# Kernel optimization log

Hardware: AMD Instinct MI355X
Metric: run time of the kernel (lower is better)

The kernel has to match this reference:

```python
import jax, jax.numpy as jnp
import numpy as np

NUM_CLIP_VIT_FEAT = 576  # default kwarg of mixed_mask


def _mixed_mask(pad_ends, full_starts, full_ends, bt2i, blm, B, S):
    # Faithful translation of OmniAttentionMechanism.mixed_mask evaluated over
    # all (b, q_idx, kv_idx). Note python operator precedence: & binds tighter
    # than ^, so the original expression is (A&t2i) ^ (B&C&lm) ^ (D&mmu).
    q_idx = jnp.arange(S)[:, None]          # [S,1]
    kv_idx = jnp.arange(S)[None, :]         # [1,S]
    causal_qk = q_idx >= kv_idx             # [S,S]
    # kv_idx < pad_ends[b, kv_idx]  ->  arange(S) < pad_ends  (per batch row)
    pad_region = jnp.arange(S) < pad_ends   # [B,S] over kv
    causal = (~pad_region)[:, None, :] & causal_qk[None]              # [B,S,S]
    # full block: kv in [full_starts[q], full_ends[q])
    full = (kv_idx < full_ends[:, None]) & (kv_idx >= full_starts[:, None])  # [S,S]
    eye = q_idx == kv_idx                                             # [S,S]
    t2i = eye[None] ^ (causal | full[None])                           # [B,S,S]
    lm = causal_qk                                                    # [S,S]
    mmu = causal_qk | (kv_idx <= NUM_CLIP_VIT_FEAT + 3)               # [S,S]
    b = jnp.arange(B)[:, None, None]
    mask = ((b < bt2i) & t2i) \
         ^ ((b >= bt2i) & (b < bt2i + blm) & lm[None]) \
         ^ ((b >= bt2i + blm) & mmu[None])
    return mask  # [B,S,S] bool


def setup_inputs() -> dict:
    key = jax.random.key(0)
    B_T2I, B_LM, B_MMU = 4, 4, 4
    B, H, S, D = B_T2I + B_LM + B_MMU, 8, 1024, 64
    k1, k2, k3 = jax.random.split(key, 3)
    q = jax.random.normal(k1, (B, H, S, D), jnp.float32)
    k = jax.random.normal(k2, (B, H, S, D), jnp.float32)
    v = jax.random.normal(k3, (B, H, S, D), jnp.float32)

    # full_starts/full_ends from image_begin_ends=[(512,1024)]
    full_starts = np.arange(S)
    full_ends = np.arange(S)
    for ib, ie in [(512, 1024)]:
        full_starts[ib:ie] = ib
        full_ends[ib:ie] = ie

    # pad_ends from default pad_begin_ends=[(0,256),(0,300),(0,400),(0,0)]
    pad_ends = np.tile(np.arange(S), (B, 1))
    for cnt, (pb, pe) in enumerate([(0, 256), (0, 300), (0, 400), (0, 0)]):
        pad_ends[cnt, pb:pe] = pe

    return {
        "q": q, "k": k, "v": v,
        "pad_ends": jnp.asarray(pad_ends, jnp.int32),
        "full_starts": jnp.asarray(full_starts, jnp.int32),
        "full_ends": jnp.asarray(full_ends, jnp.int32),
        "batch_size_t2i": B_T2I,
        "batch_size_lm": B_LM,
    }


def reference(q, k, v, pad_ends, full_starts, full_ends, batch_size_t2i, batch_size_lm):
    B, H, S, D = q.shape
    mask = _mixed_mask(pad_ends, full_starts, full_ends,
                       batch_size_t2i, batch_size_lm, B, S)      # [B,S,S]
    scale = 1.0 / jnp.sqrt(jnp.asarray(D, q.dtype))
    scores = jnp.einsum('bhqd,bhkd->bhqk', q, k) * scale          # [B,H,S,S]
    scores = jnp.where(mask[:, None], scores, jnp.asarray(-1e30, scores.dtype))
    attn = jax.nn.softmax(scores, axis=-1)
    return jnp.einsum('bhqk,bhkd->bhqd', attn, v)
```

## Files before the change

### kernel.cpp

```cpp
#include <hip/hip_runtime.h>


typedef __attribute__((ext_vector_type(8))) short short8;
typedef __attribute__((ext_vector_type(4))) float floatx4;
typedef __attribute__((ext_vector_type(4))) unsigned int uint4v;

#define S_LEN 1024
#define D_DIM 64
#define H_NUM 8
#define B_NUM 12
#define BT2I_CONST 4
#define BLM_CONST 4
#define NUM_CLIP_P3 579
#define KV_ELEMS (B_NUM * H_NUM * S_LEN * D_DIM)
#define P_EPS 7.888609052210118e-31f

__device__ __forceinline__ float bf2f(short s) {
    unsigned int u = ((unsigned int)(unsigned short)s) << 16;
    return __builtin_bit_cast(float, u);
}
__device__ __forceinline__ short f2bf(float f) {
    unsigned int u = __builtin_bit_cast(unsigned int, f);
    unsigned int r = (u + 0x7fffu + ((u >> 16) & 1u)) >> 16;
    return (short)(unsigned short)r;
}
__device__ __forceinline__ short scale_bf(short x) {
    float f = bf2f(x) * 0.125f;
    return (short)(unsigned short)(__builtin_bit_cast(unsigned int, f) >> 16);
}
__device__ __forceinline__ int detect_bf16(const unsigned int* q) {
    int l = threadIdx.x & 63;
    unsigned int w = q[l];
    unsigned int e = (w >> 7) & 0xffu;
    bool sane = (e >= 100u && e <= 140u);
    unsigned long long m = __ballot(sane);
    return (__popcll(m) > 32) ? 1 : 0;
}

__global__ __launch_bounds__(256)
void preprocess_kv(const void* __restrict__ Kv, const void* __restrict__ Vv,
                   const unsigned int* __restrict__ Qw,
                   short* __restrict__ Kf, short* __restrict__ Vf) {
    __shared__ __align__(16) short Ls[64][72];
    const int is_bf16 = detect_bf16(Qw);
    const int x = blockIdx.x;
    const int kind = x & 1;
    const int kt = (x >> 1) & 15;
    const int bh = x >> 5;
    const int t = threadIdx.x;
    const long long base = (long long)bh * S_LEN * D_DIM + (long long)kt * 64 * D_DIM;
    const void* Src = kind ? Vv : Kv;

    #pragma unroll
    for (int j = 0; j < 4; ++j) {
        int lin = j * 1024 + t * 4;
        int row = lin >> 6, col = lin & 63;
        long long src = base + (long long)row * D_DIM + col;
        short v0, v1, v2, v3;
        if (is_bf16) {
            const short* p = (const short*)Src + src;
            v0 = p[0]; v1 = p[1]; v2 = p[2]; v3 = p[3];
        } else {
            floatx4 f = *(const floatx4*)((const float*)Src + src);
            v0 = f2bf(f[0]); v1 = f2bf(f[1]); v2 = f2bf(f[2]); v3 = f2bf(f[3]);
        }
        if (kind == 0) {
            Ls[row][col] = v0; Ls[row][col + 1] = v1;
            Ls[row][col + 2] = v2; Ls[row][col + 3] = v3;
        } else {
            Ls[col][row] = v0; Ls[col + 1][row] = v1;
            Ls[col + 2][row] = v2; Ls[col + 3][row] = v3;
        }
    }
    __syncthreads();

    short* dst = (kind ? Vf : Kf) + ((long long)bh * 16 + kt) * 4096;
    #pragma unroll
    for (int rep = 0; rep < 2; ++rep) {
        int idx = rep * 256 + t;
        int g = idx >> 6, lam = idx & 63;
        int gg = g >> 1, hh = g & 1, q = lam >> 4, l16 = lam & 15;
        short8 v = *(const short8*)&Ls[gg * 16 + l16][hh * 32 + q * 8];
        *(short8*)(dst + (g * 64 + lam) * 8) = v;
    }
}

__global__ __launch_bounds__(64, 2)
void omni_attn_main(const void* __restrict__ Qv, const int* __restrict__ pad_ends,
                    const int* __restrict__ fstarts, const int* __restrict__ fends,
                    const short* __restrict__ Kf, const short* __restrict__ Vf,
                    float* __restrict__ Out) {
    const int lid = blockIdx.x;
    const int h = lid & 7;
    const int s = lid >> 3;
    const int b = s >> 6;
    const int su = s & 63;
    const int qu = (su + 5 * b) & 63;
    const int qb0 = qu * 16;

    const int t = threadIdx.x;
    const int l = t & 63;
    const int lane16 = l & 15;
    const int quad = l >> 4;

    const int is_bf16 = detect_bf16((const unsigned int*)Qv);
    const int cls = (b < BT2I_CONST) ? 0 : ((b < BT2I_CONST + BLM_CONST) ? 1 : 2);
    const int bh = b * H_NUM + h;
    const long long base = (long long)bh * S_LEN * D_DIM;
    const int qmax_blk = qb0 + 15;

    unsigned int apmask = 0u;
    int fnp = 0x7fffffff;
    if (cls == 0) {
        #pragma unroll
        for (int kt = 0; kt < 16; ++kt) {
            int kg = kt * 64 + l;
            bool nonpad = (kg >= pad_ends[b * S_LEN + kg]);
            unsigned long long m = __ballot(nonpad);
            apmask |= (m == 0ull ? 1u : 0u) << kt;
            int cand = m ? (kt * 64 + __builtin_ctzll(m)) : 0x7fffffff;
            fnp = min(fnp, cand);
        }
    }
    const bool risky = (cls == 0) && (fnp >= qb0) && (fnp <= qmax_blk);

    int fs_min, fe_max;
    {
        int fsv = fstarts[qb0 + lane16];
        int fev = fends[qb0 + lane16];
        #pragma unroll
        for (int off = 1; off < 16; off <<= 1) {
            fsv = min(fsv, __shfl_xor(fsv, off, 64));
            fev = max(fev, __shfl_xor(fev, off, 64));
        }
        fs_min = fsv; fe_max = fev;
    }

    unsigned int keepmask = 0u;
    #pragma unroll
    for (int kt = 0; kt < 16; ++kt) {
        const int kvbase = kt * 64;
        bool keep;
        if (cls == 0) {
            bool allpad = ((apmask >> kt) & 1u) != 0u;
            keep = risky ||
                   ((kvbase < fe_max) && (kvbase + 64 > fs_min)) ||
                   ((kvbase <= qmax_blk) && (!allpad || (kvbase + 63 >= qb0)));
        } else if (cls == 1) {
            keep = (kvbase <= qmax_blk);
        } else {
            keep = (kvbase <= qmax_blk) || (kvbase <= NUM_CLIP_P3);
        }
        keepmask |= (keep ? 1u : 0u) << kt;
    }

    short8 aq[2];
    {
        const int row = qb0 + lane16;
        if (is_bf16) {
            const short8* qp = (const short8*)((const short*)Qv + base
                                               + (long long)row * D_DIM + quad * 8);
            short8 r0 = qp[0], r1 = qp[4];
            #pragma unroll
            for (int jj = 0; jj < 8; ++jj) {
                aq[0][jj] = scale_bf(r0[jj]);
                aq[1][jj] = scale_bf(r1[jj]);
            }
        } else {
            const floatx4* qp = (const floatx4*)((const float*)Qv + base
                                                 + (long long)row * D_DIM + quad * 8);
            floatx4 f0 = qp[0], f1 = qp[1], f2 = qp[8], f3 = qp[9];
            #pragma unroll
            for (int jj = 0; jj < 4; ++jj) {
                aq[0][jj]     = f2bf(f0[jj] * 0.125f);
                aq[0][4 + jj] = f2bf(f1[jj] * 0.125f);
                aq[1][jj]     = f2bf(f2[jj] * 0.125f);
                aq[1][4 + jj] = f2bf(f3[jj] * 0.125f);
            }
        }
    }

    const int qvl = qb0 + lane16;
    const int fsl = fstarts[qvl];
    const int fel = fends[qvl];
    int fsmax, femin;
    {
        int a = fsl, e = fel;
        #pragma unroll
        for (int off = 1; off < 16; off <<= 1) {
            a = max(a, __shfl_xor(a, off, 64));
            e = min(e, __shfl_xor(e, off, 64));
        }
        fsmax = a; femin = e;
    }

    floatx4 Oc[4];
    float lsum = 0.f;
    #pragma unroll
    for (int c = 0; c < 4; ++c) Oc[c] = (floatx4){0.f, 0.f, 0.f, 0.f};

    const short* Kfb = Kf + (long long)bh * (16 * 4096);
    const short* Vfb = Vf + (long long)bh * (16 * 4096);

    short8 kkf[4][2];
    short8 vvf[4][2];

    auto load_K = [&](int kt) {
        const short8* p = (const short8*)(Kfb + (long long)kt * 4096);
        #pragma unroll
        for (int f = 0; f < 4; ++f)
            #pragma unroll
            for (int hh = 0; hh < 2; ++hh)
                kkf[f][hh] = p[(f * 2 + hh) * 64 + l];
    };
    auto load_V = [&](int kt) {
        const short8* p = (const short8*)(Vfb + (long long)kt * 4096);
        #pragma unroll
        for (int c = 0; c < 4; ++c)
            #pragma unroll
            for (int hh = 0; hh < 2; ++hh)
                vvf[c][hh] = p[(c * 2 + hh) * 64 + l];
    };

    unsigned int mrem = keepmask;
    int kt = __builtin_ctz(mrem); mrem &= mrem - 1;
    load_K(kt); load_V(kt);
    int pev = 0;
    if (cls == 0) pev = pad_ends[b * S_LEN + kt * 64 + l];
    for (;;) {
        int ktN = -1;
        if (mrem) { ktN = __builtin_ctz(mrem); mrem &= mrem - 1; }

        const int kvbase = kt * 64;
        unsigned long long pm = 0ull;
        if (cls == 0) {
            pm = __ballot((kvbase + l) >= pev);
            if (ktN >= 0) pev = pad_ends[b * S_LEN + ktN * 64 + l];
        }

        floatx4 sc[4];
        #pragma unroll
        for (int f = 0; f < 4; ++f) {
            floatx4 c = (floatx4){0.f, 0.f, 0.f, 0.f};
            c = __builtin_amdgcn_mfma_f32_16x16x32_bf16(kkf[f][0], aq[0], c, 0, 0, 0);
            c = __builtin_amdgcn_mfma_f32_16x16x32_bf16(kkf[f][1], aq[1], c, 0, 0, 0);
            sc[f] = c;
        }
        bool fast;
        if (cls == 0) {
            bool np_all  = (pm == ~0ull);
            bool below   = (kvbase + 63 < qb0);
            bool eyefree = below || (kvbase > qb0 + 15);
            fast = (np_all && below) ||
                   (eyefree && (kvbase >= fsmax) && (kvbase + 64 <= femin));
        } else if (cls == 1) {
            fast = (kvbase + 63 <= qb0);
        } else {
            fast = (kvbase + 63 <= qb0) || (kvbase + 63 <= NUM_CLIP_P3);
        }
        if (!fast) {
            const int q = qvl;
            #pragma unroll
            for (int f = 0; f < 4; ++f) {
                #pragma unroll
                for (int r = 0; r < 4; ++r) {
                    const int k = kvbase + f * 16 + 4 * quad + r;
                    bool m;
                    if (cls == 0) {
                        bool knp    = ((pm >> (f * 16 + 4 * quad + r)) & 1ull) != 0ull;
                        bool causal = knp && (q >= k);
                        bool full   = (k >= fsl) && (k < fel);
                        m = (q == k) != (causal || full);
                    } else if (cls == 1) {
                        m = (q >= k);
                    } else {
                        m = (q >= k) || (k <= NUM_CLIP_P3);
                    }
                    sc[f][r] = m ? sc[f][r] : -1e30f;
                }
            }
        }
        unsigned int uu[4][2];
        float ls = 0.f;
        #pragma unroll
        for (int f = 0; f < 4; ++f) {
            float p0 = __expf(sc[f][0]) + P_EPS;
            float p1 = __expf(sc[f][1]) + P_EPS;
            float p2 = __expf(sc[f][2]) + P_EPS;
            float p3 = __expf(sc[f][3]) + P_EPS;
            ls += p0 + p1 + p2 + p3;
            asm("v_cvt_pk_bf16_f32 %0, %1, %2" : "=v"(uu[f][0]) : "v"(p0), "v"(p1));
            asm("v_cvt_pk_bf16_f32 %0, %1, %2" : "=v"(uu[f][1]) : "v"(p2), "v"(p3));
        }
        lsum += ls;
        short8 pa[2];
        #pragma unroll
        for (int hh = 0; hh < 2; ++hh) {
            unsigned int x0 = uu[2 * hh][0],     y0 = uu[2 * hh + 1][0];
            unsigned int x1 = uu[2 * hh][1],     y1 = uu[2 * hh + 1][1];
            asm("v_permlane32_swap_b32 %0, %1" : "+v"(x0), "+v"(y0));
            asm("v_permlane16_swap_b32 %0, %1" : "+v"(x0), "+v"(y0));
            asm("v_permlane32_swap_b32 %0, %1" : "+v"(x1), "+v"(y1));
            asm("v_permlane16_swap_b32 %0, %1" : "+v"(x1), "+v"(y1));
            uint4v w;
            w[0] = x0; w[1] = x1; w[2] = y0; w[3] = y1;
            pa[hh] = __builtin_bit_cast(short8, w);
        }

        if (ktN >= 0) load_K(ktN);

        #pragma unroll
        for (int c = 0; c < 4; ++c) {
            Oc[c] = __builtin_amdgcn_mfma_f32_16x16x32_bf16(pa[0], vvf[c][0], Oc[c], 0, 0, 0);
            Oc[c] = __builtin_amdgcn_mfma_f32_16x16x32_bf16(pa[1], vvf[c][1], Oc[c], 0, 0, 0);
        }

        if (ktN >= 0) load_V(ktN);
        if (ktN < 0) break;
        kt = ktN;
    }

    {
        float sv0 = lsum;
        sv0 += __shfl_xor(sv0, 16, 64);
        sv0 += __shfl_xor(sv0, 32, 64);
        float* ob = Out + ((long long)bh * S_LEN + qb0) * D_DIM;
        #pragma unroll
        for (int r = 0; r < 4; ++r) {
            float sv = __shfl(sv0, quad * 4 + r, 64);
            float inv = 1.0f / sv;
            #pragma unroll
            for (int c = 0; c < 4; ++c)
                ob[(quad * 4 + r) * D_DIM + c * 16 + lane16] = Oc[c][r] * inv;
        }
    }
}

__global__ __launch_bounds__(256)
void omni_attn_fallback(const void* __restrict__ Qv, const void* __restrict__ Kv,
                        const void* __restrict__ Vv, const int* __restrict__ pad_ends,
                        const int* __restrict__ fstarts, const int* __restrict__ fends,
                        float* __restrict__ Out) {
    __shared__ short Ks[64][72];
    __shared__ short Vts[64][72];
    __shared__ short Ps[4][16][72];
    __shared__ int   padv[64];
    const int qt = blockIdx.x, h = blockIdx.y, b = blockIdx.z;
    const int t = threadIdx.x, wq = t >> 6, l = t & 63;
    const int lane16 = l & 15, quad = l >> 4;
    const int is_bf16 = detect_bf16((const unsigned int*)Qv);
    const int cls = (b < BT2I_CONST) ? 0 : ((b < BT2I_CONST + BLM_CONST) ? 1 : 2);
    const int bh = b * H_NUM + h;
    const long long base = (long long)bh * S_LEN * D_DIM;
    const short* Kb16 = (const short*)Kv + base;
    const short* Vb16 = (const short*)Vv + base;
    const float* Kbf = (const float*)Kv + base;
    const float* Vbf = (const float*)Vv + base;
    const int qbase = qt * 64 + wq * 16;
    short8 aq0, aq1;
    if (is_bf16) {
        const short8* qp = (const short8*)((const short*)Qv + base + (qbase + lane16) * D_DIM + quad * 8);
        short8 r0 = qp[0], r1 = qp[4];
        #pragma unroll
        for (int jj = 0; jj < 8; ++jj) { aq0[jj] = scale_bf(r0[jj]); aq1[jj] = scale_bf(r1[jj]); }
    } else {
        const floatx4* qp = (const floatx4*)((const float*)Qv + base + (qbase + lane16) * D_DIM + quad * 8);
        floatx4 f0 = qp[0], f1 = qp[1], f2 = qp[8], f3 = qp[9];
        #pragma unroll
        for (int jj = 0; jj < 4; ++jj) {
            aq0[jj] = f2bf(f0[jj] * 0.125f); aq0[4 + jj] = f2bf(f1[jj] * 0.125f);
            aq1[jj] = f2bf(f2[jj] * 0.125f); aq1[4 + jj] = f2bf(f3[jj] * 0.125f);
        }
    }
    int qg[4], fs[4], fe[4];
    #pragma unroll
    for (int r = 0; r < 4; ++r) {
        qg[r] = qbase + quad * 4 + r; fs[r] = fstarts[qg[r]]; fe[r] = fends[qg[r]];
    }
    floatx4 Oc[4];
    #pragma unroll
    for (int c = 0; c < 4; ++c) Oc[c] = (floatx4){0.f, 0.f, 0.f, 0.f};
    float m_i[4] = {-1e30f, -1e30f, -1e30f, -1e30f};
    float l_i[4] = {0.f, 0.f, 0.f, 0.f};
    for (int kt = 0; kt < S_LEN / 64; ++kt) {
        const int kvbase = kt * 64;
        __syncthreads();
        {
            const int kvr = t >> 2, seg = t & 3;
            if (is_bf16) {
                const short8* gk = (const short8*)(Kb16 + (kvbase + kvr) * D_DIM);
                *(short8*)&Ks[kvr][seg * 8] = gk[seg];
                *(short8*)&Ks[kvr][(seg + 4) * 8] = gk[seg + 4];
                const short8* gv = (const short8*)(Vb16 + (kvbase + kvr) * D_DIM);
                short8 v0 = gv[seg], v1 = gv[seg + 4];
                #pragma unroll
                for (int jj = 0; jj < 8; ++jj) {
                    Vts[seg * 8 + jj][kvr] = v0[jj];
                    Vts[32 + seg * 8 + jj][kvr] = v1[jj];
                }
            } else {
                const floatx4* gk = (const floatx4*)(Kbf + (kvbase + kvr) * D_DIM);
                floatx4 k0 = gk[seg * 2], k1 = gk[seg * 2 + 1];
                floatx4 k2 = gk[8 + seg * 2], k3 = gk[8 + seg * 2 + 1];
                #pragma unroll
                for (int jj = 0; jj < 4; ++jj) {
                    Ks[kvr][seg * 8 + jj] = f2bf(k0[jj]);
                    Ks[kvr][seg * 8 + 4 + jj] = f2bf(k1[jj]);
                    Ks[kvr][32 + seg * 8 + jj] = f2bf(k2[jj]);
                    Ks[kvr][32 + seg * 8 + 4 + jj] = f2bf(k3[jj]);
                }
                const floatx4* gv = (const floatx4*)(Vbf + (kvbase + kvr) * D_DIM);
                floatx4 v0 = gv[seg * 2], v1 = gv[seg * 2 + 1];
                floatx4 v2 = gv[8 + seg * 2], v3 = gv[8 + seg * 2 + 1];
                #pragma unroll
                for (int jj = 0; jj < 4; ++jj) {
                    Vts[seg * 8 + jj][kvr] = f2bf(v0[jj]);
                    Vts[seg * 8 + 4 + jj][kvr] = f2bf(v1[jj]);
                    Vts[32 + seg * 8 + jj][kvr] = f2bf(v2[jj]);
                    Vts[32 + seg * 8 + 4 + jj][kvr] = f2bf(v3[jj]);
                }
            }
            if (t < 64) {
                int kg = kvbase + t;
                padv[t] = (kg < pad_ends[b * S_LEN + kg]) ? 1 : 0;
            }
        }
        __syncthreads();
        floatx4 sc[4];
        #pragma unroll
        for (int f = 0; f < 4; ++f) {
            short8 b0 = *(const short8*)&Ks[f * 16 + lane16][quad * 8];
            short8 b1 = *(const short8*)&Ks[f * 16 + lane16][32 + quad * 8];
            floatx4 c = (floatx4){0.f, 0.f, 0.f, 0.f};
            c = __builtin_amdgcn_mfma_f32_16x16x32_bf16(aq0, b0, c, 0, 0, 0);
            c = __builtin_amdgcn_mfma_f32_16x16x32_bf16(aq1, b1, c, 0, 0, 0);
            sc[f] = c;
        }
        int col[4], cpad[4];
        #pragma unroll
        for (int f = 0; f < 4; ++f) {
            col[f] = kvbase + f * 16 + lane16;
            cpad[f] = padv[f * 16 + lane16];
        }
        if (cls == 0) {
            #pragma unroll
            for (int r = 0; r < 4; ++r) {
                const int q = qg[r];
                #pragma unroll
                for (int f = 0; f < 4; ++f) {
                    const int k = col[f];
                    bool causal = (!cpad[f]) && (q >= k);
                    bool full = (k >= fs[r]) && (k < fe[r]);
                    bool m = (q == k) != (causal || full);
                    sc[f][r] = m ? sc[f][r] : -1e30f;
                }
            }
        } else if (cls == 1) {
            #pragma unroll
            for (int r = 0; r < 4; ++r) {
                const int q = qg[r];
                #pragma unroll
                for (int f = 0; f < 4; ++f)
                    sc[f][r] = (q >= col[f]) ? sc[f][r] : -1e30f;
            }
        } else {
            #pragma unroll
            for (int r = 0; r < 4; ++r) {
                const int q = qg[r];
                #pragma unroll
                for (int f = 0; f < 4; ++f) {
                    bool m = (q >= col[f]) || (col[f] <= NUM_CLIP_P3);
                    sc[f][r] = m ? sc[f][r] : -1e30f;
                }
            }
        }
        #pragma unroll
        for (int r = 0; r < 4; ++r) {
            float rmax = fmaxf(fmaxf(sc[0][r], sc[1][r]), fmaxf(sc[2][r], sc[3][r]));
            #pragma unroll
            for (int off = 1; off < 16; off <<= 1)
                rmax = fmaxf(rmax, __shfl_xor(rmax, off, 64));
            float mnew = fmaxf(m_i[r], rmax);
            float alpha = __expf(m_i[r] - mnew);
            m_i[r] = mnew;
            float psum = 0.f;
            #pragma unroll
            for (int f = 0; f < 4; ++f) {
                float p = __expf(sc[f][r] - mnew);
                sc[f][r] = p; psum += p;
            }
            #pragma unroll
            for (int off = 1; off < 16; off <<= 1)
                psum += __shfl_xor(psum, off, 64);
            l_i[r] = l_i[r] * alpha + psum;
            Oc[0][r] *= alpha; Oc[1][r] *= alpha; Oc[2][r] *= alpha; Oc[3][r] *= alpha;
        }
        #pragma unroll
        for (int r = 0; r < 4; ++r)
            #pragma unroll
            for (int f = 0; f < 4; ++f)
                Ps[wq][quad * 4 + r][f * 16 + lane16] = f2bf(sc[f][r]);
        __syncthreads();
        short8 a0 = *(const short8*)&Ps[wq][lane16][quad * 8];
        short8 a1 = *(const short8*)&Ps[wq][lane16][32 + quad * 8];
        #pragma unroll
        for (int c = 0; c < 4; ++c) {
            short8 b0 = *(const short8*)&Vts[c * 16 + lane16][quad * 8];
            short8 b1 = *(const short8*)&Vts[c * 16 + lane16][32 + quad * 8];
            Oc[c] = __builtin_amdgcn_mfma_f32_16x16x32_bf16(a0, b0, Oc[c], 0, 0, 0);
            Oc[c] = __builtin_amdgcn_mfma_f32_16x16x32_bf16(a1, b1, Oc[c], 0, 0, 0);
        }
    }
    float* ob = Out + ((long long)bh * S_LEN + qbase) * D_DIM;
    #pragma unroll
    for (int r = 0; r < 4; ++r) {
        float inv = 1.0f / l_i[r];
        #pragma unroll
        for (int c = 0; c < 4; ++c)
            ob[(quad * 4 + r) * D_DIM + c * 16 + lane16] = Oc[c][r] * inv;
    }
}

extern "C" void kernel_launch(void* const* d_in, const int* in_sizes, int n_in,
                              void* d_out, int out_size, void* d_ws, size_t ws_size,
                              hipStream_t stream) {
    const void* Q = d_in[0];
    const void* K = d_in[1];
    const void* V = d_in[2];
    const int* pad_ends = (const int*)d_in[3];
    const int* fstarts  = (const int*)d_in[4];
    const int* fends    = (const int*)d_in[5];
    float* Out = (float*)d_out;

    const size_t need = 2 * (size_t)KV_ELEMS * 2;

    if (ws_size >= need) {
        short* Kf = (short*)d_ws;
        short* Vf = Kf + KV_ELEMS;
        preprocess_kv<<<3072, 256, 0, stream>>>(K, V, (const unsigned int*)Q, Kf, Vf);
        omni_attn_main<<<6144, 64, 0, stream>>>(Q, pad_ends, fstarts, fends,
                                                Kf, Vf, Out);
    } else {
        dim3 grid(S_LEN / 64, H_NUM, B_NUM);
        omni_attn_fallback<<<grid, 256, 0, stream>>>(Q, K, V, pad_ends, fstarts,
                                                     fends, Out);
    }
}
```

Measured before the change: 165.3 us.

## Use per-XCD persistent atomic work queue with longest-first tile ordering

Replaces the fixed one-block-per-tile grid with persistent blocks that pull work items from an atomic counter per XCD. Each XCD is tied to one head through blockIdx & 7, and items are ordered so the heaviest query tiles (high query index, all batches) are issued first, to reduce tail imbalance from uneven causal and mask work. The counters are zeroed inside the preprocessing kernel, and the next K-tile prefetch now starts before the mask evaluation. This adds atomic traffic and relies on blocks being dispatched round-robin across XCDs for locality; results stay correct either way.

```diff
diff --git a/kernel.cpp b/kernel.cpp
--- a/kernel.cpp
+++ b/kernel.cpp
@@ -14,6 +14,7 @@
 #define NUM_CLIP_P3 579
 #define KV_ELEMS (B_NUM * H_NUM * S_LEN * D_DIM)
 #define P_EPS 7.888609052210118e-31f
+#define ITEMS_PER_XCD 768
 
 __device__ __forceinline__ float bf2f(short s) {
     unsigned int u = ((unsigned int)(unsigned short)s) << 16;
@@ -40,7 +41,8 @@
 __global__ __launch_bounds__(256)
 void preprocess_kv(const void* __restrict__ Kv, const void* __restrict__ Vv,
                    const unsigned int* __restrict__ Qw,
-                   short* __restrict__ Kf, short* __restrict__ Vf) {
+                   short* __restrict__ Kf, short* __restrict__ Vf,
+                   unsigned int* __restrict__ cnts) {
     __shared__ __align__(16) short Ls[64][72];
     const int is_bf16 = detect_bf16(Qw);
     const int x = blockIdx.x;
@@ -48,6 +50,7 @@
     const int kt = (x >> 1) & 15;
     const int bh = x >> 5;
     const int t = threadIdx.x;
+    if (x == 0 && t < 128) cnts[t] = 0u;
     const long long base = (long long)bh * S_LEN * D_DIM + (long long)kt * 64 * D_DIM;
     const void* Src = kind ? Vv : Kv;
 
@@ -89,14 +92,11 @@
 void omni_attn_main(const void* __restrict__ Qv, const int* __restrict__ pad_ends,
                     const int* __restrict__ fstarts, const int* __restrict__ fends,
                     const short* __restrict__ Kf, const short* __restrict__ Vf,
+                    unsigned int* __restrict__ cnts,
                     float* __restrict__ Out) {
-    const int lid = blockIdx.x;
-    const int h = lid & 7;
-    const int s = lid >> 3;
-    const int b = s >> 6;
-    const int su = s & 63;
-    const int qu = (su + 5 * b) & 63;
-    const int qb0 = qu * 16;
+    const int xcd = blockIdx.x & 7;
+    const int h = xcd;
+    unsigned int* cnt = cnts + xcd * 16;
 
     const int t = threadIdx.x;
     const int l = t & 63;
@@ -104,234 +104,252 @@
     const int quad = l >> 4;
 
     const int is_bf16 = detect_bf16((const unsigned int*)Qv);
-    const int cls = (b < BT2I_CONST) ? 0 : ((b < BT2I_CONST + BLM_CONST) ? 1 : 2);
-    const int bh = b * H_NUM + h;
-    const long long base = (long long)bh * S_LEN * D_DIM;
-    const int qmax_blk = qb0 + 15;
-
-    unsigned int apmask = 0u;
-    int fnp = 0x7fffffff;
-    if (cls == 0) {
+
+    for (;;) {
+        int w;
+        {
+            int wl = 0;
+            if (l == 0) wl = (int)atomicAdd(cnt, 1u);
+            w = __shfl(wl, 0, 64);
+        }
+        if (w >= ITEMS_PER_XCD) break;
+
+        int b, qu;
+        if (w < 336)      { qu = 63 - w / 12; b = w % 12; }
+        else if (w < 480) { int i = w - 336; qu = 35 - (i >> 2); b = 8 + (i & 3); }
+        else              { int i = w - 480; qu = 35 - (i >> 3); b = i & 7; }
+        const int qb0 = qu * 16;
+
+        const int cls = (b < BT2I_CONST) ? 0 : ((b < BT2I_CONST + BLM_CONST) ? 1 : 2);
+        const int bh = b * H_NUM + h;
+        const long long base = (long long)bh * S_LEN * D_DIM;
+        const int qmax_blk = qb0 + 15;
+
+        unsigned int apmask = 0u;
+        int fnp = 0x7fffffff;
+        if (cls == 0) {
+            #pragma unroll
+            for (int kt = 0; kt < 16; ++kt) {
+                int kg = kt * 64 + l;
+                bool nonpad = (kg >= pad_ends[b * S_LEN + kg]);
+                unsigned long long m = __ballot(nonpad);
+                apmask |= (m == 0ull ? 1u : 0u) << kt;
+                int cand = m ? (kt * 64 + __builtin_ctzll(m)) : 0x7fffffff;
+                fnp = min(fnp, cand);
+            }
+        }
+        const bool risky = (cls == 0) && (fnp >= qb0) && (fnp <= qmax_blk);
+
+        int fs_min, fe_max;
+        {
+            int fsv = fstarts[qb0 + lane16];
+            int fev = fends[qb0 + lane16];
+            #pragma unroll
+            for (int off = 1; off < 16; off <<= 1) {
+                fsv = min(fsv, __shfl_xor(fsv, off, 64));
+                fev = max(fev, __shfl_xor(fev, off, 64));
+            }
+            fs_min = fsv; fe_max = fev;
+        }
+
+        unsigned int keepmask = 0u;
         #pragma unroll
         for (int kt = 0; kt < 16; ++kt) {
-            int kg = kt * 64 + l;
-            bool nonpad = (kg >= pad_ends[b * S_LEN + kg]);
-            unsigned long long m = __ballot(nonpad);
-            apmask |= (m == 0ull ? 1u : 0u) << kt;
-            int cand = m ? (kt * 64 + __builtin_ctzll(m)) : 0x7fffffff;
-            fnp = min(fnp, cand);
-        }
-    }
-    const bool risky = (cls == 0) && (fnp >= qb0) && (fnp <= qmax_blk);
-
-    int fs_min, fe_max;
-    {
-        int fsv = fstarts[qb0 + lane16];
-        int fev = fends[qb0 + lane16];
-        #pragma unroll
-        for (int off = 1; off < 16; off <<= 1) {
-            fsv = min(fsv, __shfl_xor(fsv, off, 64));
-            fev = max(fev, __shfl_xor(fev, off, 64));
-        }
-        fs_min = fsv; fe_max = fev;
-    }
-
-    unsigned int keepmask = 0u;
-    #pragma unroll
-    for (int kt = 0; kt < 16; ++kt) {
-        const int kvbase = kt * 64;
-        bool keep;
-        if (cls == 0) {
-            bool allpad = ((apmask >> kt) & 1u) != 0u;
-            keep = risky ||
-                   ((kvbase < fe_max) && (kvbase + 64 > fs_min)) ||
-                   ((kvbase <= qmax_blk) && (!allpad || (kvbase + 63 >= qb0)));
-        } else if (cls == 1) {
-            keep = (kvbase <= qmax_blk);
-        } else {
-            keep = (kvbase <= qmax_blk) || (kvbase <= NUM_CLIP_P3);
-        }
-        keepmask |= (keep ? 1u : 0u) << kt;
-    }
-
-    short8 aq[2];
-    {
-        const int row = qb0 + lane16;
-        if (is_bf16) {
-            const short8* qp = (const short8*)((const short*)Qv + base
-                                               + (long long)row * D_DIM + quad * 8);
-            short8 r0 = qp[0], r1 = qp[4];
-            #pragma unroll
-            for (int jj = 0; jj < 8; ++jj) {
-                aq[0][jj] = scale_bf(r0[jj]);
-                aq[1][jj] = scale_bf(r1[jj]);
-            }
-        } else {
-            const floatx4* qp = (const floatx4*)((const float*)Qv + base
-                                                 + (long long)row * D_DIM + quad * 8);
-            floatx4 f0 = qp[0], f1 = qp[1], f2 = qp[8], f3 = qp[9];
-            #pragma unroll
-            for (int jj = 0; jj < 4; ++jj) {
-                aq[0][jj]     = f2bf(f0[jj] * 0.125f);
-                aq[0][4 + jj] = f2bf(f1[jj] * 0.125f);
-                aq[1][jj]     = f2bf(f2[jj] * 0.125f);
-                aq[1][4 + jj] = f2bf(f3[jj] * 0.125f);
-            }
-        }
-    }
-
-    const int qvl = qb0 + lane16;
-    const int fsl = fstarts[qvl];
-    const int fel = fends[qvl];
-    int fsmax, femin;
-    {
-        int a = fsl, e = fel;
-        #pragma unroll
-        for (int off = 1; off < 16; off <<= 1) {
-            a = max(a, __shfl_xor(a, off, 64));
-            e = min(e, __shfl_xor(e, off, 64));
-        }
-        fsmax = a; femin = e;
-    }
-
-    floatx4 Oc[4];
-    float lsum = 0.f;
-    #pragma unroll
-    for (int c = 0; c < 4; ++c) Oc[c] = (floatx4){0.f, 0.f, 0.f, 0.f};
-
-    const short* Kfb = Kf + (long long)bh * (16 * 4096);
-    const short* Vfb = Vf + (long long)bh * (16 * 4096);
-
-    short8 kkf[4][2];
-    short8 vvf[4][2];
-
-    auto load_K = [&](int kt) {
-        const short8* p = (const short8*)(Kfb + (long long)kt * 4096);
-        #pragma unroll
-        for (int f = 0; f < 4; ++f)
-            #pragma unroll
-            for (int hh = 0; hh < 2; ++hh)
-                kkf[f][hh] = p[(f * 2 + hh) * 64 + l];
-    };
-    auto load_V = [&](int kt) {
-        const short8* p = (const short8*)(Vfb + (long long)kt * 4096);
-        #pragma unroll
-        for (int c = 0; c < 4; ++c)
-            #pragma unroll
-            for (int hh = 0; hh < 2; ++hh)
-                vvf[c][hh] = p[(c * 2 + hh) * 64 + l];
-    };
-
-    unsigned int mrem = keepmask;
-    int kt = __builtin_ctz(mrem); mrem &= mrem - 1;
-    load_K(kt); load_V(kt);
-    int pev = 0;
-    if (cls == 0) pev = pad_ends[b * S_LEN + kt * 64 + l];
-    for (;;) {
-        int ktN = -1;
-        if (mrem) { ktN = __builtin_ctz(mrem); mrem &= mrem - 1; }
-
-        const int kvbase = kt * 64;
-        unsigned long long pm = 0ull;
-        if (cls == 0) {
-            pm = __ballot((kvbase + l) >= pev);
-            if (ktN >= 0) pev = pad_ends[b * S_LEN + ktN * 64 + l];
-        }
-
-        floatx4 sc[4];
-        #pragma unroll
-        for (int f = 0; f < 4; ++f) {
-            floatx4 c = (floatx4){0.f, 0.f, 0.f, 0.f};
-            c = __builtin_amdgcn_mfma_f32_16x16x32_bf16(kkf[f][0], aq[0], c, 0, 0, 0);
-            c = __builtin_amdgcn_mfma_f32_16x16x32_bf16(kkf[f][1], aq[1], c, 0, 0, 0);
-            sc[f] = c;
-        }
-        bool fast;
-        if (cls == 0) {
-            bool np_all  = (pm == ~0ull);
-            bool below   = (kvbase + 63 < qb0);
-            bool eyefree = below || (kvbase > qb0 + 15);
-            fast = (np_all && below) ||
-                   (eyefree && (kvbase >= fsmax) && (kvbase + 64 <= femin));
-        } else if (cls == 1) {
-            fast = (kvbase + 63 <= qb0);
-        } else {
-            fast = (kvbase + 63 <= qb0) || (kvbase + 63 <= NUM_CLIP_P3);
-        }
-        if (!fast) {
-            const int q = qvl;
+            const int kvbase = kt * 64;
+            bool keep;
+            if (cls == 0) {
+                bool allpad = ((apmask >> kt) & 1u) != 0u;
+                keep = risky ||
+                       ((kvbase < fe_max) && (kvbase + 64 > fs_min)) ||
+                       ((kvbase <= qmax_blk) && (!allpad || (kvbase + 63 >= qb0)));
+            } else if (cls == 1) {
+                keep = (kvbase <= qmax_blk);
+            } else {
+                keep = (kvbase <= qmax_blk) || (kvbase <= NUM_CLIP_P3);
+            }
+            keepmask |= (keep ? 1u : 0u) << kt;
+        }
+
+        short8 aq[2];
+        {
+            const int row = qb0 + lane16;
+            if (is_bf16) {
+                const short8* qp = (const short8*)((const short*)Qv + base
+                                                   + (long long)row * D_DIM + quad * 8);
+                short8 r0 = qp[0], r1 = qp[4];
+                #pragma unroll
+                for (int jj = 0; jj < 8; ++jj) {
+                    aq[0][jj] = scale_bf(r0[jj]);
+                    aq[1][jj] = scale_bf(r1[jj]);
+                }
+            } else {
+                const floatx4* qp = (const floatx4*)((const float*)Qv + base
+                                                     + (long long)row * D_DIM + quad * 8);
+                floatx4 f0 = qp[0], f1 = qp[1], f2 = qp[8], f3 = qp[9];
+                #pragma unroll
+                for (int jj = 0; jj < 4; ++jj) {
+                    aq[0][jj]     = f2bf(f0[jj] * 0.125f);
+                    aq[0][4 + jj] = f2bf(f1[jj] * 0.125f);
+                    aq[1][jj]     = f2bf(f2[jj] * 0.125f);
+                    aq[1][4 + jj] = f2bf(f3[jj] * 0.125f);
+                }
+            }
+        }
+
+        const int qvl = qb0 + lane16;
+        const int fsl = fstarts[qvl];
+        const int fel = fends[qvl];
+        int fsmax, femin;
+        {
+            int a = fsl, e = fel;
+            #pragma unroll
+            for (int off = 1; off < 16; off <<= 1) {
+                a = max(a, __shfl_xor(a, off, 64));
+                e = min(e, __shfl_xor(e, off, 64));
+            }
+            fsmax = a; femin = e;
+        }
+
+        floatx4 Oc[4];
+        float lsum = 0.f;
+        #pragma unroll
+        for (int c = 0; c < 4; ++c) Oc[c] = (floatx4){0.f, 0.f, 0.f, 0.f};
+
+        const short* Kfb = Kf + (long long)bh * (16 * 4096);
+        const short* Vfb = Vf + (long long)bh * (16 * 4096);
+
+        short8 kkf[4][2];
+        short8 vvf[4][2];
+
+        auto load_K = [&](int kt) {
+            const short8* p = (const short8*)(Kfb + (long long)kt * 4096);
+            #pragma unroll
+            for (int f = 0; f < 4; ++f)
+                #pragma unroll
+                for (int hh = 0; hh < 2; ++hh)
+                    kkf[f][hh] = p[(f * 2 + hh) * 64 + l];
+        };
+        auto load_V = [&](int kt) {
+            const short8* p = (const short8*)(Vfb + (long long)kt * 4096);
+            #pragma unroll
+            for (int c = 0; c < 4; ++c)
+                #pragma unroll
+                for (int hh = 0; hh < 2; ++hh)
+                    vvf[c][hh] = p[(c * 2 + hh) * 64 + l];
+        };
+
+        unsigned int mrem = keepmask;
+        int kt = __builtin_ctz(mrem); mrem &= mrem - 1;
+        load_K(kt); load_V(kt);
+        int pev = 0;
+        if (cls == 0) pev = pad_ends[b * S_LEN + kt * 64 + l];
+        for (;;) {
+            int ktN = -1;
+            if (mrem) { ktN = __builtin_ctz(mrem); mrem &= mrem - 1; }
+
+            const int kvbase = kt * 64;
+            unsigned long long pm = 0ull;
+            if (cls == 0) {
+                pm = __ballot((kvbase + l) >= pev);
+                if (ktN >= 0) pev = pad_ends[b * S_LEN + ktN * 64 + l];
+            }
+
+            floatx4 sc[4];
             #pragma unroll
             for (int f = 0; f < 4; ++f) {
-                #pragma unroll
-                for (int r = 0; r < 4; ++r) {
-                    const int k = kvbase + f * 16 + 4 * quad + r;
-                    bool m;
-                    if (cls == 0) {
-                        bool knp    = ((pm >> (f * 16 + 4 * quad + r)) & 1ull) != 0ull;
-                        bool causal = knp && (q >= k);
-                        bool full   = (k >= fsl) && (k < fel);
-                        m = (q == k) != (causal || full);
-                    } else if (cls == 1) {
-                        m = (q >= k);
-                    } else {
-                        m = (q >= k) || (k <= NUM_CLIP_P3);
+                floatx4 c = (floatx4){0.f, 0.f, 0.f, 0.f};
+                c = __builtin_amdgcn_mfma_f32_16x16x32_bf16(kkf[f][0], aq[0], c, 0, 0, 0);
+                c = __builtin_amdgcn_mfma_f32_16x16x32_bf16(kkf[f][1], aq[1], c, 0, 0, 0);
+                sc[f] = c;
+            }
+
+            if (ktN >= 0) load_K(ktN);
+
+            bool fast;
+            if (cls == 0) {
+                bool np_all  = (pm == ~0ull);
+                bool below   = (kvbase + 63 < qb0);
+                bool eyefree = below || (kvbase > qb0 + 15);
+                fast = (np_all && below) ||
+                       (eyefree && (kvbase >= fsmax) && (kvbase + 64 <= femin));
+            } else if (cls == 1) {
+                fast = (kvbase + 63 <= qb0);
+            } else {
+                fast = (kvbase + 63 <= qb0) || (kvbase + 63 <= NUM_CLIP_P3);
+            }
+            if (!fast) {
+                const int q = qvl;
+                #pragma unroll
+                for (int f = 0; f < 4; ++f) {
+                    #pragma unroll
+                    for (int r = 0; r < 4; ++r) {
+                        const int k = kvbase + f * 16 + 4 * quad + r;
+                        bool m;
+                        if (cls == 0) {
+                            bool knp    = ((pm >> (f * 16 + 4 * quad + r)) & 1ull) != 0ull;
+                            bool causal = knp && (q >= k);
+                            bool full   = (k >= fsl) && (k < fel);
+                            m = (q == k) != (causal || full);
+                        } else if (cls == 1) {
+                            m = (q >= k);
+                        } else {
+                            m = (q >= k) || (k <= NUM_CLIP_P3);
+                        }
+                        sc[f][r] = m ? sc[f][r] : -1e30f;
                     }
-                    sc[f][r] = m ? sc[f][r] : -1e30f;
-                }
-            }
-        }
-        unsigned int uu[4][2];
-        float ls = 0.f;
-        #pragma unroll
-        for (int f = 0; f < 4; ++f) {
-            float p0 = __expf(sc[f][0]) + P_EPS;
-            float p1 = __expf(sc[f][1]) + P_EPS;
-            float p2 = __expf(sc[f][2]) + P_EPS;
-            float p3 = __expf(sc[f][3]) + P_EPS;
-            ls += p0 + p1 + p2 + p3;
-            asm("v_cvt_pk_bf16_f32 %0, %1, %2" : "=v"(uu[f][0]) : "v"(p0), "v"(p1));
-            asm("v_cvt_pk_bf16_f32 %0, %1, %2" : "=v"(uu[f][1]) : "v"(p2), "v"(p3));
-        }
-        lsum += ls;
-        short8 pa[2];
-        #pragma unroll
-        for (int hh = 0; hh < 2; ++hh) {
-            unsigned int x0 = uu[2 * hh][0],     y0 = uu[2 * hh + 1][0];
-            unsigned int x1 = uu[2 * hh][1],     y1 = uu[2 * hh + 1][1];
-            asm("v_permlane32_swap_b32 %0, %1" : "+v"(x0), "+v"(y0));
-            asm("v_permlane16_swap_b32 %0, %1" : "+v"(x0), "+v"(y0));
-            asm("v_permlane32_swap_b32 %0, %1" : "+v"(x1), "+v"(y1));
-            asm("v_permlane16_swap_b32 %0, %1" : "+v"(x1), "+v"(y1));
-            uint4v w;
-            w[0] = x0; w[1] = x1; w[2] = y0; w[3] = y1;
-            pa[hh] = __builtin_bit_cast(short8, w);
-        }
-
-        if (ktN >= 0) load_K(ktN);
-
-        #pragma unroll
-        for (int c = 0; c < 4; ++c) {
-            Oc[c] = __builtin_amdgcn_mfma_f32_16x16x32_bf16(pa[0], vvf[c][0], Oc[c], 0, 0, 0);
-            Oc[c] = __builtin_amdgcn_mfma_f32_16x16x32_bf16(pa[1], vvf[c][1], Oc[c], 0, 0, 0);
-        }
-
-        if (ktN >= 0) load_V(ktN);
-        if (ktN < 0) break;
-        kt = ktN;
-    }
-
-    {
-        float sv0 = lsum;
-        sv0 += __shfl_xor(sv0, 16, 64);
-        sv0 += __shfl_xor(sv0, 32, 64);
-        float* ob = Out + ((long long)bh * S_LEN + qb0) * D_DIM;
-        #pragma unroll
-        for (int r = 0; r < 4; ++r) {
-            float sv = __shfl(sv0, quad * 4 + r, 64);
-            float inv = 1.0f / sv;
-            #pragma unroll
-            for (int c = 0; c < 4; ++c)
-                ob[(quad * 4 + r) * D_DIM + c * 16 + lane16] = Oc[c][r] * inv;
+                }
+            }
+            unsigned int uu[4][2];
+            float ls = 0.f;
+            #pragma unroll
+            for (int f = 0; f < 4; ++f) {
+                float p0 = __expf(sc[f][0]) + P_EPS;
+                float p1 = __expf(sc[f][1]) + P_EPS;
+                float p2 = __expf(sc[f][2]) + P_EPS;
+                float p3 = __expf(sc[f][3]) + P_EPS;
+                ls += p0 + p1 + p2 + p3;
+                asm("v_cvt_pk_bf16_f32 %0, %1, %2" : "=v"(uu[f][0]) : "v"(p0), "v"(p1));
+                asm("v_cvt_pk_bf16_f32 %0, %1, %2" : "=v"(uu[f][1]) : "v"(p2), "v"(p3));
+            }
+            lsum += ls;
+            short8 pa[2];
+            #pragma unroll
+            for (int hh = 0; hh < 2; ++hh) {
+                unsigned int x0 = uu[2 * hh][0],     y0 = uu[2 * hh + 1][0];
+                unsigned int x1 = uu[2 * hh][1],     y1 = uu[2 * hh + 1][1];
+                asm("v_permlane32_swap_b32 %0, %1" : "+v"(x0), "+v"(y0));
+                asm("v_permlane16_swap_b32 %0, %1" : "+v"(x0), "+v"(y0));
+                asm("v_permlane32_swap_b32 %0, %1" : "+v"(x1), "+v"(y1));
+                asm("v_permlane16_swap_b32 %0, %1" : "+v"(x1), "+v"(y1));
+                uint4v ww;
+                ww[0] = x0; ww[1] = x1; ww[2] = y0; ww[3] = y1;
+                pa[hh] = __builtin_bit_cast(short8, ww);
+            }
+
+            #pragma unroll
+            for (int c = 0; c < 4; ++c) {
+                Oc[c] = __builtin_amdgcn_mfma_f32_16x16x32_bf16(pa[0], vvf[c][0], Oc[c], 0, 0, 0);
+                Oc[c] = __builtin_amdgcn_mfma_f32_16x16x32_bf16(pa[1], vvf[c][1], Oc[c], 0, 0, 0);
+            }
+
+            if (ktN >= 0) load_V(ktN);
+            if (ktN < 0) break;
+            kt = ktN;
+        }
+
+        {
+            float sv0 = lsum;
+            sv0 += __shfl_xor(sv0, 16, 64);
+            sv0 += __shfl_xor(sv0, 32, 64);
+            float* ob = Out + ((long long)bh * S_LEN + qb0) * D_DIM;
+            #pragma unroll
+            for (int r = 0; r < 4; ++r) {
+                float sv = __shfl(sv0, quad * 4 + r, 64);
+                float inv = 1.0f / sv;
+                #pragma unroll
+                for (int c = 0; c < 4; ++c)
+                    ob[(quad * 4 + r) * D_DIM + c * 16 + lane16] = Oc[c][r] * inv;
+            }
         }
     }
 }
@@ -532,14 +550,16 @@
     const int* fends    = (const int*)d_in[5];
     float* Out = (float*)d_out;
 
-    const size_t need = 2 * (size_t)KV_ELEMS * 2;
+    const size_t need = 2 * (size_t)KV_ELEMS * 2 + 512;
 
     if (ws_size >= need) {
         short* Kf = (short*)d_ws;
         short* Vf = Kf + KV_ELEMS;
-        preprocess_kv<<<3072, 256, 0, stream>>>(K, V, (const unsigned int*)Q, Kf, Vf);
-        omni_attn_main<<<6144, 64, 0, stream>>>(Q, pad_ends, fstarts, fends,
-                                                Kf, Vf, Out);
+        unsigned int* cnts = (unsigned int*)(Vf + KV_ELEMS);
+        preprocess_kv<<<3072, 256, 0, stream>>>(K, V, (const unsigned int*)Q,
+                                                Kf, Vf, cnts);
+        omni_attn_main<<<4096, 64, 0, stream>>>(Q, pad_ends, fstarts, fends,
+                                                Kf, Vf, cnts, Out);
     } else {
         dim3 grid(S_LEN / 64, H_NUM, B_NUM);
         omni_attn_fallback<<<grid, 256, 0, stream>>>(Q, K, V, pad_ends, fstarts,
```

Result: slower. 197.0 us (+19.1%).
